# Performance work log

Hardware: AMD Instinct MI355X
Metric: run time of the kernel (lower is better)

## Reference

```python
import jax, jax.numpy as jnp
import numpy as np

INV_SQRT2 = 0.7071067811865476
SCALES = 3


def dwt_analysis(x, dec_lo, dec_hi, scales):
    """Multi-level 1D DWT along last axis (pywt/ptwt convention).
    x: [B, D]. dec_lo/dec_hi are cross-correlation filters (torch conv1d
    semantics, i.e. the flipped pywt decomposition filters as stored by the
    repo). Returns [cA_s | cD_s | ... | cD_1] truncated to the last D columns
    (identity for Haar on power-of-two D)."""
    flen = dec_lo.shape[0]
    pad = (2 * flen - 3) // 2  # ptwt zero-pad; 0 for Haar (flen=2)
    filt = jnp.stack([dec_lo, dec_hi])[:, None, :]  # [2, 1, flen]
    lo = x[:, None, :]  # [B, 1, D]
    highs = []
    for _ in range(scales):
        out = jax.lax.conv_general_dilated(
            lo, filt, window_strides=(2,), padding=[(pad, pad)],
            dimension_numbers=('NCH', 'OIH', 'NCH'))  # [B, 2, D/2]
        lo = out[:, 0:1, :]
        highs.append(out[:, 1, :])
    coeffs = jnp.concatenate([lo[:, 0, :]] + highs[::-1], axis=-1)
    return coeffs[:, -x.shape[-1]:]


def setup_inputs() -> dict:
    key = jax.random.key(0)
    k1, k2, k3, k4, k5 = jax.random.split(key, 5)
    B, D = 4096, 4096
    x = jax.random.normal(k1, (B, D), jnp.float32)
    diag_s = jax.random.normal(k2, (D,), jnp.float32)
    diag_g = jax.random.normal(k3, (D,), jnp.float32)
    diag_b = jax.random.normal(k4, (D,), jnp.float32)
    perm = jax.random.permutation(k5, jnp.arange(D))  # random column permutation
    # Haar analysis filters in cross-correlation (torch conv1d) orientation
    dec_lo = jnp.array([INV_SQRT2, INV_SQRT2], jnp.float32)
    dec_hi = jnp.array([INV_SQRT2, -INV_SQRT2], jnp.float32)
    return {"x": x, "diag_s": diag_s, "diag_g": diag_g, "diag_b": diag_b,
            "dec_lo": dec_lo, "dec_hi": dec_hi, "perm": perm, "scales": SCALES}


def reference(x, diag_s, diag_g, diag_b, dec_lo, dec_hi, perm, scales):
    # mul_b: x @ diag(b) == columnwise scale (same math, no O(d^2) matmul)
    h = x * diag_b
    h = dwt_analysis(h, dec_lo, dec_hi, scales)
    # mul_p: x @ P for a permutation matrix == column gather
    h = jnp.take(h, perm, axis=1)
    h = h * diag_g  # mul_g
    h = dwt_analysis(h, dec_lo, dec_hi, scales)
    return h * diag_s  # mul_s
```

## Files before the change

### kernel.cpp

```cpp
#include <hip/hip_runtime.h>


#define D   4096
#define NT  256
#define R   4

#define C_INV_SQRT2 0.70710678118654752440f

typedef float vf2 __attribute__((ext_vector_type(2)));
typedef float vf4 __attribute__((ext_vector_type(4)));

static __device__ __forceinline__ int swz(int i) {
    return i ^ ((i >> 5) & 31);
}

static __device__ __forceinline__ void dwt3_reg(const float v[16],
                                                float a3[2], float d3[2],
                                                float d2[4], float d1[8]) {
    float a1[8];
    #pragma unroll
    for (int j = 0; j < 8; ++j) {
        a1[j] = (v[2 * j] + v[2 * j + 1]) * C_INV_SQRT2;
        d1[j] = (v[2 * j] - v[2 * j + 1]) * C_INV_SQRT2;
    }
    float a2[4];
    #pragma unroll
    for (int j = 0; j < 4; ++j) {
        a2[j] = (a1[2 * j] + a1[2 * j + 1]) * C_INV_SQRT2;
        d2[j] = (a1[2 * j] - a1[2 * j + 1]) * C_INV_SQRT2;
    }
    #pragma unroll
    for (int j = 0; j < 2; ++j) {
        a3[j] = (a2[2 * j] + a2[2 * j + 1]) * C_INV_SQRT2;
        d3[j] = (a2[2 * j] - a2[2 * j + 1]) * C_INV_SQRT2;
    }
}

__global__ __launch_bounds__(NT) void wavelet_rows_kernel(
    const float* __restrict__ x,
    const float* __restrict__ diag_s,
    const float* __restrict__ diag_g,
    const float* __restrict__ diag_b,
    const int*   __restrict__ perm,
    float*       __restrict__ out)
{
    __shared__ float buf[2][D];

    const int t = threadIdx.x;
    const size_t row0 = (size_t)blockIdx.x * R;

    float db[16], dg[16];
    int   pidx[16];
    {
        const vf4* b4 = (const vf4*)diag_b;
        const vf4* g4 = (const vf4*)diag_g;
        const int4* p4 = (const int4*)perm;
        #pragma unroll
        for (int k = 0; k < 4; ++k) {
            vf4 bv = b4[4 * t + k];
            db[4 * k + 0] = bv.x; db[4 * k + 1] = bv.y;
            db[4 * k + 2] = bv.z; db[4 * k + 3] = bv.w;
            vf4 gv = g4[4 * t + k];
            dg[4 * k + 0] = gv.x; dg[4 * k + 1] = gv.y;
            dg[4 * k + 2] = gv.z; dg[4 * k + 3] = gv.w;
            int4 pv = p4[4 * t + k];
            pidx[4 * k + 0] = pv.x; pidx[4 * k + 1] = pv.y;
            pidx[4 * k + 2] = pv.z; pidx[4 * k + 3] = pv.w;
        }
    }
    vf2 sA, sD3;
    vf4 sD2, sD1a, sD1b;
    {
        const vf2* s2 = (const vf2*)diag_s;
        const vf4* s4 = (const vf4*)diag_s;
        sA   = s2[t];
        sD3  = s2[256 + t];
        sD2  = s4[256 + t];
        sD1a = s4[512 + 2 * t];
        sD1b = s4[512 + 2 * t + 1];
    }

    for (int r = 0; r < R; ++r) {
        float* b = buf[r & 1];
        const vf4* x4 = (const vf4*)(x + (row0 + r) * (size_t)D);

        float v[16];
        #pragma unroll
        for (int k = 0; k < 4; ++k) {
            vf4 xv = x4[4 * t + k];
            v[4 * k + 0] = xv.x * db[4 * k + 0];
            v[4 * k + 1] = xv.y * db[4 * k + 1];
            v[4 * k + 2] = xv.z * db[4 * k + 2];
            v[4 * k + 3] = xv.w * db[4 * k + 3];
        }

        float a3[2], d3[2], d2[4], d1[8];
        dwt3_reg(v, a3, d3, d2, d1);

        #pragma unroll
        for (int j = 0; j < 2; ++j) b[swz(2 * t + j)]        = a3[j];
        #pragma unroll
        for (int j = 0; j < 2; ++j) b[swz(512 + 2 * t + j)]  = d3[j];
        #pragma unroll
        for (int j = 0; j < 4; ++j) b[swz(1024 + 4 * t + j)] = d2[j];
        #pragma unroll
        for (int j = 0; j < 8; ++j) b[swz(2048 + 8 * t + j)] = d1[j];

        __syncthreads();

        float w[16];
        #pragma unroll
        for (int k = 0; k < 16; ++k) {
            w[k] = b[swz(pidx[k])] * dg[k];
        }

        float b3[2], e3[2], e2[4], e1[8];
        dwt3_reg(w, b3, e3, e2, e1);

        float* orow = out + (row0 + r) * (size_t)D;
        {
            vf2* o2 = (vf2*)orow;
            vf2 ov;
            ov.x = b3[0] * sA.x;  ov.y = b3[1] * sA.y;
            __builtin_nontemporal_store(ov, &o2[t]);
            ov.x = e3[0] * sD3.x; ov.y = e3[1] * sD3.y;
            __builtin_nontemporal_store(ov, &o2[256 + t]);

            vf4* o4 = (vf4*)orow;
            vf4 o;
            o.x = e2[0] * sD2.x; o.y = e2[1] * sD2.y;
            o.z = e2[2] * sD2.z; o.w = e2[3] * sD2.w;
            __builtin_nontemporal_store(o, &o4[256 + t]);
            o.x = e1[0] * sD1a.x; o.y = e1[1] * sD1a.y;
            o.z = e1[2] * sD1a.z; o.w = e1[3] * sD1a.w;
            __builtin_nontemporal_store(o, &o4[512 + 2 * t]);
            o.x = e1[4] * sD1b.x; o.y = e1[5] * sD1b.y;
            o.z = e1[6] * sD1b.z; o.w = e1[7] * sD1b.w;
            __builtin_nontemporal_store(o, &o4[512 + 2 * t + 1]);
        }
    }
}

extern "C" void kernel_launch(void* const* d_in, const int* in_sizes, int n_in,
                              void* d_out, int out_size, void* d_ws, size_t ws_size,
                              hipStream_t stream) {
    const float* x      = (const float*)d_in[0];
    const float* diag_s = (const float*)d_in[1];
    const float* diag_g = (const float*)d_in[2];
    const float* diag_b = (const float*)d_in[3];
    const int* perm     = (const int*)d_in[6];
    float* out          = (float*)d_out;

    const int B = 4096 / R;
    wavelet_rows_kernel<<<B, NT, 0, stream>>>(x, diag_s, diag_g, diag_b, perm, out);
}
```

Measured before the change: 129.3 us.

## Prefetch next row into registers, single LDS buffer, reload diag_s per row

Software-prefetches the next row of x into registers before the current row's wavelet transform, so global load latency overlaps with compute. The LDS buffer shrinks from two rows to one, with a second barrier added per row to protect it. diag_s is now reloaded from global (cached) memory for every row instead of held in registers, and the nontemporal output stores become plain stores. Together these aim to hide load latency and lower register and LDS pressure, at the cost of an extra barrier and extra cache reads.

```diff
diff --git a/kernel.cpp b/kernel.cpp
--- a/kernel.cpp
+++ b/kernel.cpp
@@ -44,7 +44,7 @@
     const int*   __restrict__ perm,
     float*       __restrict__ out)
 {
-    __shared__ float buf[2][D];
+    __shared__ float buf[D];
 
     const int t = threadIdx.x;
     const size_t row0 = (size_t)blockIdx.x * R;
@@ -68,75 +68,82 @@
             pidx[4 * k + 2] = pv.z; pidx[4 * k + 3] = pv.w;
         }
     }
-    vf2 sA, sD3;
-    vf4 sD2, sD1a, sD1b;
+
+    vf4 xv[4];
     {
-        const vf2* s2 = (const vf2*)diag_s;
-        const vf4* s4 = (const vf4*)diag_s;
-        sA   = s2[t];
-        sD3  = s2[256 + t];
-        sD2  = s4[256 + t];
-        sD1a = s4[512 + 2 * t];
-        sD1b = s4[512 + 2 * t + 1];
+        const vf4* x4 = (const vf4*)(x + row0 * (size_t)D);
+        #pragma unroll
+        for (int k = 0; k < 4; ++k) xv[k] = x4[4 * t + k];
     }
 
     for (int r = 0; r < R; ++r) {
-        float* b = buf[r & 1];
-        const vf4* x4 = (const vf4*)(x + (row0 + r) * (size_t)D);
-
         float v[16];
         #pragma unroll
         for (int k = 0; k < 4; ++k) {
-            vf4 xv = x4[4 * t + k];
-            v[4 * k + 0] = xv.x * db[4 * k + 0];
-            v[4 * k + 1] = xv.y * db[4 * k + 1];
-            v[4 * k + 2] = xv.z * db[4 * k + 2];
-            v[4 * k + 3] = xv.w * db[4 * k + 3];
+            v[4 * k + 0] = xv[k].x * db[4 * k + 0];
+            v[4 * k + 1] = xv[k].y * db[4 * k + 1];
+            v[4 * k + 2] = xv[k].z * db[4 * k + 2];
+            v[4 * k + 3] = xv[k].w * db[4 * k + 3];
+        }
+
+        if (r + 1 < R) {
+            const vf4* xn = (const vf4*)(x + (row0 + r + 1) * (size_t)D);
+            #pragma unroll
+            for (int k = 0; k < 4; ++k) xv[k] = xn[4 * t + k];
         }
 
         float a3[2], d3[2], d2[4], d1[8];
         dwt3_reg(v, a3, d3, d2, d1);
 
         #pragma unroll
-        for (int j = 0; j < 2; ++j) b[swz(2 * t + j)]        = a3[j];
+        for (int j = 0; j < 2; ++j) buf[swz(2 * t + j)]        = a3[j];
         #pragma unroll
-        for (int j = 0; j < 2; ++j) b[swz(512 + 2 * t + j)]  = d3[j];
+        for (int j = 0; j < 2; ++j) buf[swz(512 + 2 * t + j)]  = d3[j];
         #pragma unroll
-        for (int j = 0; j < 4; ++j) b[swz(1024 + 4 * t + j)] = d2[j];
+        for (int j = 0; j < 4; ++j) buf[swz(1024 + 4 * t + j)] = d2[j];
         #pragma unroll
-        for (int j = 0; j < 8; ++j) b[swz(2048 + 8 * t + j)] = d1[j];
+        for (int j = 0; j < 8; ++j) buf[swz(2048 + 8 * t + j)] = d1[j];
 
         __syncthreads();
 
         float w[16];
         #pragma unroll
         for (int k = 0; k < 16; ++k) {
-            w[k] = b[swz(pidx[k])] * dg[k];
+            w[k] = buf[swz(pidx[k])] * dg[k];
         }
+
+        __syncthreads();
 
         float b3[2], e3[2], e2[4], e1[8];
         dwt3_reg(w, b3, e3, e2, e1);
 
         float* orow = out + (row0 + r) * (size_t)D;
         {
+            const vf2* s2 = (const vf2*)diag_s;
             vf2* o2 = (vf2*)orow;
-            vf2 ov;
-            ov.x = b3[0] * sA.x;  ov.y = b3[1] * sA.y;
-            __builtin_nontemporal_store(ov, &o2[t]);
-            ov.x = e3[0] * sD3.x; ov.y = e3[1] * sD3.y;
-            __builtin_nontemporal_store(ov, &o2[256 + t]);
+            vf2 sv, ov;
+            sv = s2[t];
+            ov.x = b3[0] * sv.x; ov.y = b3[1] * sv.y;
+            o2[t] = ov;
+            sv = s2[256 + t];
+            ov.x = e3[0] * sv.x; ov.y = e3[1] * sv.y;
+            o2[256 + t] = ov;
 
+            const vf4* s4 = (const vf4*)diag_s;
             vf4* o4 = (vf4*)orow;
-            vf4 o;
-            o.x = e2[0] * sD2.x; o.y = e2[1] * sD2.y;
-            o.z = e2[2] * sD2.z; o.w = e2[3] * sD2.w;
-            __builtin_nontemporal_store(o, &o4[256 + t]);
-            o.x = e1[0] * sD1a.x; o.y = e1[1] * sD1a.y;
-            o.z = e1[2] * sD1a.z; o.w = e1[3] * sD1a.w;
-            __builtin_nontemporal_store(o, &o4[512 + 2 * t]);
-            o.x = e1[4] * sD1b.x; o.y = e1[5] * sD1b.y;
-            o.z = e1[6] * sD1b.z; o.w = e1[7] * sD1b.w;
-            __builtin_nontemporal_store(o, &o4[512 + 2 * t + 1]);
+            vf4 sw, o;
+            sw = s4[256 + t];
+            o.x = e2[0] * sw.x; o.y = e2[1] * sw.y;
+            o.z = e2[2] * sw.z; o.w = e2[3] * sw.w;
+            o4[256 + t] = o;
+            sw = s4[512 + 2 * t];
+            o.x = e1[0] * sw.x; o.y = e1[1] * sw.y;
+            o.z = e1[2] * sw.z; o.w = e1[3] * sw.w;
+            o4[512 + 2 * t] = o;
+            sw = s4[512 + 2 * t + 1];
+            o.x = e1[4] * sw.x; o.y = e1[5] * sw.y;
+            o.z = e1[6] * sw.z; o.w = e1[7] * sw.w;
+            o4[512 + 2 * t + 1] = o;
         }
     }
 }
```

Result: no change. 131.7 us (+1.9%).
